# Kernel optimization log

Hardware: AMD Instinct MI355X
Metric: run time of the kernel (lower is better)

## Reference

```python
import jax, jax.numpy as jnp
import numpy as np

B, S, H, NH, HD = 2, 2048, 2048, 16, 128
E, TOPK, I = 8, 2, 2048
EPS = 1e-5
ROPE_THETA = 10000.0


def setup_inputs() -> dict:
    key = jax.random.key(0)
    ks = jax.random.split(key, 11)
    s = 0.02
    return {
        "hidden_states": jax.random.normal(ks[0], (B, S, H), jnp.float32),
        "position_ids": jnp.broadcast_to(jnp.arange(S, dtype=jnp.int32), (B, S)),
        "rms1_w": jnp.ones((H,), jnp.float32),
        "rms2_w": jnp.ones((H,), jnp.float32),
        "q_w": jax.random.normal(ks[1], (H, H), jnp.float32) * s,
        "k_w": jax.random.normal(ks[2], (H, H), jnp.float32) * s,
        "v_w": jax.random.normal(ks[3], (H, H), jnp.float32) * s,
        "o_w": jax.random.normal(ks[4], (H, H), jnp.float32) * s,
        "router_w": jax.random.normal(ks[5], (H, E), jnp.float32) * s,
        "w1": jax.random.normal(ks[6], (E, H, I), jnp.float32) * s,
        "w2": jax.random.normal(ks[7], (E, I, H), jnp.float32) * s,
        "w3": jax.random.normal(ks[8], (E, H, I), jnp.float32) * s,
    }


def rmsnorm(x, w):
    var = jnp.mean(x * x, axis=-1, keepdims=True)
    return (x * jax.lax.rsqrt(var + EPS)) * w


def rope(x, pos):
    # x: [B,S,NH,HD], pos: [B,S]
    half = HD // 2
    inv_freq = 1.0 / (ROPE_THETA ** (jnp.arange(0, half, dtype=jnp.float32) / half))
    ang = pos.astype(jnp.float32)[..., None] * inv_freq  # [B,S,half]
    cos = jnp.cos(ang)[:, :, None, :]
    sin = jnp.sin(ang)[:, :, None, :]
    x1, x2 = x[..., :half], x[..., half:]
    return jnp.concatenate([x1 * cos - x2 * sin, x2 * cos + x1 * sin], axis=-1)


def attention(x, pos, q_w, k_w, v_w, o_w):
    q = (x @ q_w).reshape(B, S, NH, HD)
    k = (x @ k_w).reshape(B, S, NH, HD)
    v = (x @ v_w).reshape(B, S, NH, HD)
    q = rope(q, pos)
    k = rope(k, pos)
    scores = jnp.einsum("bqhd,bkhd->bhqk", q, k) / np.sqrt(HD).astype(np.float32)
    causal = jnp.tril(jnp.ones((S, S), bool))
    scores = jnp.where(causal, scores, jnp.finfo(scores.dtype).min)
    probs = jax.nn.softmax(scores, axis=-1)
    ctx = jnp.einsum("bhqk,bkhd->bqhd", probs, v).reshape(B, S, H)
    return ctx @ o_w


def moe(x, router_w, w1, w2, w3):
    t = x.reshape(B * S, H)
    probs = jax.nn.softmax(t @ router_w, axis=-1)  # [T,E]
    top_v, top_i = jax.lax.top_k(probs, TOPK)
    top_v = top_v / jnp.sum(top_v, axis=-1, keepdims=True)
    T = B * S
    coeff = jnp.zeros((T, E), x.dtype).at[jnp.arange(T)[:, None], top_i].set(top_v)
    y = jnp.zeros((T, H), x.dtype)
    for e in range(E):  # fixed small expert loop
        h = jax.nn.silu(t @ w1[e]) * (t @ w3[e])
        y = y + coeff[:, e:e + 1] * (h @ w2[e])
    return y.reshape(B, S, H)


def reference(hidden_states, position_ids, rms1_w, rms2_w, q_w, k_w, v_w, o_w,
              router_w, w1, w2, w3):
    residual = hidden_states
    h = rmsnorm(hidden_states, rms1_w).astype(hidden_states.dtype)
    h = attention(h, position_ids, q_w, k_w, v_w, o_w)
    h = residual + h
    residual = h
    h = rmsnorm(h, rms2_w).astype(h.dtype)
    h = moe(h, router_w, w1, w2, w3)
    return residual + h
```

## Files before the change

kernel.cpp:

```cpp
#include <hip/hip_runtime.h>
#include <hip/hip_bf16.h>

constexpr int CB   = 2;
constexpr int CS   = 2048;
constexpr int CH   = 2048;
constexpr int CNH  = 16;
constexpr int CHD  = 128;
constexpr int CE   = 8;
constexpr int CI   = 2048;
constexpr int CT   = CB * CS;
constexpr int CQK  = 4096;

typedef __attribute__((ext_vector_type(8))) short short8;
typedef __attribute__((ext_vector_type(4))) float float4v;
typedef __attribute__((ext_vector_type(4))) unsigned short ushort4v;
typedef unsigned int uint32;

__device__ __forceinline__ float bf2f(unsigned short u) {
    union { unsigned int i; float f; } x; x.i = ((unsigned int)u) << 16; return x.f;
}
__device__ __forceinline__ unsigned short f2bf(float f) {
    union { float f; unsigned int i; } x; x.f = f;
    unsigned int r = x.i + 0x7fffu + ((x.i >> 16) & 1u);
    return (unsigned short)(r >> 16);
}
__device__ __forceinline__ uint32 packpair(uint32 r0, uint32 r1) {
    return __builtin_amdgcn_perm(r1, r0, 0x07060302u);
}
__device__ __forceinline__ uint32 rnebits(float f) {
    uint32 u = __float_as_uint(f);
    return u + 0x7fffu + ((u >> 16) & 1u);
}
__device__ __forceinline__ void split2(float f0, float f1, uint32& h, uint32& l) {
    uint32 r0 = rnebits(f0), r1 = rnebits(f1);
    h = packpair(r0, r1);
    float d0 = f0 - __uint_as_float(r0 & 0xffff0000u);
    float d1 = f1 - __uint_as_float(r1 & 0xffff0000u);
    l = packpair(rnebits(d0), rnebits(d1));
}
__device__ __forceinline__ void rne16_store(const float* fv, unsigned short* dst) {
    uint32 h[8];
    #pragma unroll
    for (int p = 0; p < 8; p++) h[p] = packpair(rnebits(fv[2 * p]), rnebits(fv[2 * p + 1]));
    ((uint4*)dst)[0] = make_uint4(h[0], h[1], h[2], h[3]);
    ((uint4*)dst)[1] = make_uint4(h[4], h[5], h[6], h[7]);
}
__device__ __forceinline__ void gl16(const void* g, void* l) {
    __builtin_amdgcn_global_load_lds(
        (const __attribute__((address_space(1))) void*)g,
        (__attribute__((address_space(3))) void*)l, 16, 0, 0);
}

__global__ __launch_bounds__(256) void rmsnorm_k(const float* __restrict__ x,
                                                 const float* __restrict__ w,
                                                 unsigned short* __restrict__ o1,
                                                 unsigned short* __restrict__ o2) {
    const int row = blockIdx.x;
    const float* xr = x + (size_t)row * CH;
    const int base = threadIdx.x * 8;
    float4 v0 = *(const float4*)(xr + base);
    float4 v1 = *(const float4*)(xr + base + 4);
    float ss = v0.x*v0.x + v0.y*v0.y + v0.z*v0.z + v0.w*v0.w
             + v1.x*v1.x + v1.y*v1.y + v1.z*v1.z + v1.w*v1.w;
    #pragma unroll
    for (int o = 1; o < 64; o <<= 1) ss += __shfl_xor(ss, o);
    __shared__ float ps[4];
    if ((threadIdx.x & 63) == 0) ps[threadIdx.x >> 6] = ss;
    __syncthreads();
    const float scale = rsqrtf((ps[0] + ps[1] + ps[2] + ps[3]) / (float)CH + 1e-5f);
    float4 w0 = *(const float4*)(w + base);
    float4 w1 = *(const float4*)(w + base + 4);
    float r[8] = {v0.x * scale * w0.x, v0.y * scale * w0.y, v0.z * scale * w0.z, v0.w * scale * w0.w,
                  v1.x * scale * w1.x, v1.y * scale * w1.y, v1.z * scale * w1.z, v1.w * scale * w1.w};
    uint32 h[4], l[4];
    #pragma unroll
    for (int p = 0; p < 4; p++) split2(r[2 * p], r[2 * p + 1], h[p], l[p]);
    *(uint4*)(o1 + (size_t)row * CH + base) = make_uint4(h[0], h[1], h[2], h[3]);
    *(uint4*)(o2 + (size_t)row * CH + base) = make_uint4(l[0], l[1], l[2], l[3]);
}

__global__ __launch_bounds__(256) void rmsrouter_k(const float* __restrict__ x,
                                                   const float* __restrict__ w,
                                                   const float* __restrict__ rw,
                                                   unsigned short* __restrict__ h2,
                                                   int* __restrict__ cnt,
                                                   int* __restrict__ tok,
                                                   float* __restrict__ gate) {
    const int row = blockIdx.x;
    const float* xr = x + (size_t)row * CH;
    const int base = threadIdx.x * 8;
    float4 v0 = *(const float4*)(xr + base);
    float4 v1 = *(const float4*)(xr + base + 4);
    float ss = v0.x*v0.x + v0.y*v0.y + v0.z*v0.z + v0.w*v0.w
             + v1.x*v1.x + v1.y*v1.y + v1.z*v1.z + v1.w*v1.w;
    #pragma unroll
    for (int o = 1; o < 64; o <<= 1) ss += __shfl_xor(ss, o);
    __shared__ float ps[4];
    __shared__ double dacc[4][8];
    const int wave = threadIdx.x >> 6, lane = threadIdx.x & 63;
    if (lane == 0) ps[wave] = ss;
    __syncthreads();
    const float scale = rsqrtf((ps[0] + ps[1] + ps[2] + ps[3]) / (float)CH + 1e-5f);
    float4 w0 = *(const float4*)(w + base);
    float4 w1 = *(const float4*)(w + base + 4);
    float r[8] = {v0.x * scale * w0.x, v0.y * scale * w0.y, v0.z * scale * w0.z, v0.w * scale * w0.w,
                  v1.x * scale * w1.x, v1.y * scale * w1.y, v1.z * scale * w1.z, v1.w * scale * w1.w};
    rne16_store(r, h2 + (size_t)row * CH + base);
    const float vv[8] = {v0.x, v0.y, v0.z, v0.w, v1.x, v1.y, v1.z, v1.w};
    const float ww[8] = {w0.x, w0.y, w0.z, w0.w, w1.x, w1.y, w1.z, w1.w};
    double acc[8] = {0, 0, 0, 0, 0, 0, 0, 0};
    #pragma unroll
    for (int jj = 0; jj < 8; jj++) {
        const double xn = (double)vv[jj] * (double)ww[jj];
        const float* rr = rw + (size_t)(base + jj) * CE;
        #pragma unroll
        for (int e = 0; e < 8; e++) acc[e] += xn * (double)rr[e];
    }
    #pragma unroll
    for (int e = 0; e < 8; e++) {
        #pragma unroll
        for (int o = 1; o < 64; o <<= 1) acc[e] += __shfl_xor(acc[e], o);
    }
    if (lane == 0) {
        #pragma unroll
        for (int e = 0; e < 8; e++) dacc[wave][e] = acc[e];
    }
    __syncthreads();
    if (threadIdx.x == 0) {
        double a[8];
        #pragma unroll
        for (int e = 0; e < 8; e++) a[e] = dacc[0][e] + dacc[1][e] + dacc[2][e] + dacc[3][e];
        int e0 = 0;
        #pragma unroll
        for (int e = 1; e < 8; e++) if (a[e] > a[e0]) e0 = e;
        int e1 = (e0 == 0) ? 1 : 0;
        #pragma unroll
        for (int e = 0; e < 8; e++) if (e != e0 && a[e] > a[e1]) e1 = e;
        const double dl = (double)scale * (a[e1] - a[e0]);
        const double p1r = exp(dl);
        const float g0 = (float)(1.0 / (1.0 + p1r));
        const float g1 = (float)(p1r / (1.0 + p1r));
        int pos0 = atomicAdd(&cnt[e0], 1);
        tok[e0 * 4096 + pos0] = row; gate[e0 * 4096 + pos0] = g0;
        int pos1 = atomicAdd(&cnt[e1], 1);
        tok[e1 * 4096 + pos1] = row; gate[e1 * 4096 + pos1] = g1;
    }
}

__global__ void rope_tab_k(float2* __restrict__ tab) {
    int i = blockIdx.x * 256 + threadIdx.x;
    int p = i >> 6, j = i & 63;
    double inv = pow(10000.0, -(double)j / 64.0);
    float invf = (float)inv;
    float angf = (float)p * invf;
    double da = (double)angf;
    tab[i] = make_float2((float)cos(da), (float)sin(da));
}

__global__ __launch_bounds__(256) void rope_k(unsigned short* __restrict__ qh,
                                              unsigned short* __restrict__ ql,
                                              const int* __restrict__ pos,
                                              const float2* __restrict__ tab) {
    int i = blockIdx.x * 256 + threadIdx.x;
    if (i >= CT * CNH * 8) return;
    int t = i >> 7, r = i & 127, hh = r >> 3, jo = (r & 7) << 3;
    const float2* tp = tab + (size_t)pos[t] * 64 + jo;
    float4 tc0 = ((const float4*)tp)[0];
    float4 tc1 = ((const float4*)tp)[1];
    float4 tc2 = ((const float4*)tp)[2];
    float4 tc3 = ((const float4*)tp)[3];
    float cx[8] = {tc0.x, tc0.z, tc1.x, tc1.z, tc2.x, tc2.z, tc3.x, tc3.z};
    float cy[8] = {tc0.y, tc0.w, tc1.y, tc1.w, tc2.y, tc2.w, tc3.y, tc3.w};
    const size_t off = (size_t)t * CQK + hh * CHD + jo;
    #pragma unroll
    for (int s = 0; s < 2; s++) {
        unsigned short* hp = qh + off + s * CH;
        unsigned short* lp = ql + off + s * CH;
        short8 x1h = *(short8*)hp,        x1l = *(short8*)lp;
        short8 x2h = *(short8*)(hp + 64), x2l = *(short8*)(lp + 64);
        const unsigned short* p1h = (const unsigned short*)&x1h;
        const unsigned short* p1l = (const unsigned short*)&x1l;
        const unsigned short* p2h = (const unsigned short*)&x2h;
        const unsigned short* p2l = (const unsigned short*)&x2l;
        short8 y1h, y1l, y2h, y2l;
        unsigned short* q1h = (unsigned short*)&y1h;
        unsigned short* q1l = (unsigned short*)&y1l;
        unsigned short* q2h = (unsigned short*)&y2h;
        unsigned short* q2l = (unsigned short*)&y2l;
        #pragma unroll
        for (int jj = 0; jj < 8; jj++) {
            const float x1 = bf2f(p1h[jj]) + bf2f(p1l[jj]);
            const float x2 = bf2f(p2h[jj]) + bf2f(p2l[jj]);
            const float yy1 = x1 * cx[jj] - x2 * cy[jj];
            const float yy2 = x2 * cx[jj] + x1 * cy[jj];
            const uint32 r1 = rnebits(yy1), r2 = rnebits(yy2);
            q1h[jj] = (unsigned short)(r1 >> 16);
            q2h[jj] = (unsigned short)(r2 >> 16);
            q1l[jj] = f2bf(yy1 - __uint_as_float(r1 & 0xffff0000u));
            q2l[jj] = f2bf(yy2 - __uint_as_float(r2 & 0xffff0000u));
        }
        *(short8*)hp        = y1h;
        *(short8*)(hp + 64) = y2h;
        *(short8*)lp        = y1l;
        *(short8*)(lp + 64) = y2l;
    }
}

template<int NMAT>
__global__ __launch_bounds__(256) void conv_k(const float* __restrict__ S0,
                                              const float* __restrict__ S1,
                                              unsigned short* __restrict__ D) {
    __shared__ float t[64][65];
    const int n0 = blockIdx.x * 64, k0 = blockIdx.y * 64, e = blockIdx.z;
    const size_t esrc = (size_t)e * 2048 * 2048;
    const int cc = threadIdx.x & 63, r4 = threadIdx.x >> 6;
    const int nl = threadIdx.x >> 2, q = threadIdx.x & 3;
    #pragma unroll
    for (int s = 0; s < NMAT; s++) {
        const float* S = s ? S1 : S0;
        __syncthreads();
        #pragma unroll
        for (int j = 0; j < 16; j++) {
            const int row = j * 4 + r4;
            t[cc][row] = S[esrc + (size_t)(k0 + row) * 2048 + n0 + cc];
        }
        __syncthreads();
        const int orow = (NMAT == 2) ? (2 * (n0 + nl) + s) : (n0 + nl);
        unsigned short* dp = D + (size_t)e * (NMAT * 2048) * 2048 + (size_t)orow * 2048 + k0 + q * 16;
        float fv[16];
        #pragma unroll
        for (int j = 0; j < 16; j++) fv[j] = t[nl][q * 16 + j];
        rne16_store(fv, dp);
    }
}

template<int NMAT>
__global__ __launch_bounds__(256) void convs_k(const float* __restrict__ S0,
                                               const float* __restrict__ S1,
                                               const float* __restrict__ S2,
                                               unsigned short* __restrict__ Dh,
                                               unsigned short* __restrict__ Dl) {
    __shared__ float t[64][65];
    const int n0 = blockIdx.x * 64, k0 = blockIdx.y * 64, z = blockIdx.z;
    const float* S = S0;
    if (NMAT == 3) S = (z == 0) ? S0 : ((z == 1) ? S1 : S2);
    const int cc = threadIdx.x & 63, r4 = threadIdx.x >> 6;
    #pragma unroll
    for (int j = 0; j < 16; j++) {
        const int row = j * 4 + r4;
        t[cc][row] = S[(size_t)(k0 + row) * 2048 + n0 + cc];
    }
    __syncthreads();
    const int nl = threadIdx.x >> 2, q = threadIdx.x & 3;
    float fv[16];
    #pragma unroll
    for (int j = 0; j < 16; j++) fv[j] = t[nl][q * 16 + j];
    uint32 h[8], l[8];
    #pragma unroll
    for (int p = 0; p < 8; p++) split2(fv[2 * p], fv[2 * p + 1], h[p], l[p]);
    const size_t off = (size_t)(z * 2048 + n0 + nl) * 2048 + k0 + q * 16;
    ((uint4*)(Dh + off))[0] = make_uint4(h[0], h[1], h[2], h[3]);
    ((uint4*)(Dh + off))[1] = make_uint4(h[4], h[5], h[6], h[7]);
    ((uint4*)(Dl + off))[0] = make_uint4(l[0], l[1], l[2], l[3]);
    ((uint4*)(Dl + off))[1] = make_uint4(l[4], l[5], l[6], l[7]);
}

template<int MODE>
__global__ __launch_bounds__(256) void sgemm_k(
    const unsigned short* __restrict__ Ahg, const unsigned short* __restrict__ Alg, int lda,
    const unsigned short* __restrict__ Bhg, const unsigned short* __restrict__ Blg, int K,
    unsigned short* __restrict__ Ch, unsigned short* __restrict__ Cl,
    float* __restrict__ Cf, int ldc,
    const float* __restrict__ resid, float* __restrict__ C2,
    unsigned short* __restrict__ Vh, unsigned short* __restrict__ Vl) {
    __shared__ unsigned short SS[2][4][128 * 32];
    const int mt = blockIdx.x, nt = blockIdx.y, tid = threadIdx.x;
    const int m0 = mt * 128;
    const int wave = tid >> 6, lane = tid & 63;
    const int lr = lane & 15, lg = lane >> 4;
    const int wr = (tid >> 7) & 1, wc = (tid >> 6) & 1;
    const int sr = lane >> 2;
    const int sc = (lane & 3) * 8;
    const int r0 = wave * 32;
    const int lofs = r0 * 32;
    const unsigned short* gAh = Ahg + (size_t)(m0 + r0 + sr) * lda + sc;
    const unsigned short* gAl = Alg + (size_t)(m0 + r0 + sr) * lda + sc;
    const unsigned short* gBh = Bhg + (size_t)(nt * 128 + r0 + sr) * K + sc;
    const unsigned short* gBl = Blg + (size_t)(nt * 128 + r0 + sr) * K + sc;
    const size_t rstepA = (size_t)16 * lda, rstepB = (size_t)16 * K;

    float4v acc[4][4];
    #pragma unroll
    for (int m = 0; m < 4; m++)
        #pragma unroll
        for (int n = 0; n < 4; n++) acc[m][n] = (float4v){0.f, 0.f, 0.f, 0.f};

    gl16(gAh, &SS[0][0][lofs]);           gl16(gAh + rstepA, &SS[0][0][lofs + 512]);
    gl16(gAl, &SS[0][1][lofs]);           gl16(gAl + rstepA, &SS[0][1][lofs + 512]);
    gl16(gBh, &SS[0][2][lofs]);           gl16(gBh + rstepB, &SS[0][2][lofs + 512]);
    gl16(gBl, &SS[0][3][lofs]);           gl16(gBl + rstepB, &SS[0][3][lofs + 512]);
    __syncthreads();

    int cur = 0;
    for (int k0 = 0; k0 < K; k0 += 32) {
        if (k0 + 32 < K) {
            const int nb = cur ^ 1;
            const int kn = k0 + 32;
            gl16(gAh + kn, &SS[nb][0][lofs]);          gl16(gAh + kn + rstepA, &SS[nb][0][lofs + 512]);
            gl16(gAl + kn, &SS[nb][1][lofs]);          gl16(gAl + kn + rstepA, &SS[nb][1][lofs + 512]);
            gl16(gBh + kn, &SS[nb][2][lofs]);          gl16(gBh + kn + rstepB, &SS[nb][2][lofs + 512]);
            gl16(gBl + kn, &SS[nb][3][lofs]);          gl16(gBl + kn + rstepB, &SS[nb][3][lofs + 512]);
        }
        const unsigned short* PAh = SS[cur][0];
        const unsigned short* PAl = SS[cur][1];
        const unsigned short* PBh = SS[cur][2];
        const unsigned short* PBl = SS[cur][3];
        short8 fah[4], fal[4], fbh[4], fbl[4];
        #pragma unroll
        for (int m = 0; m < 4; m++) {
            fah[m] = *(const short8*)(PAh + (wr * 64 + m * 16 + lr) * 32 + lg * 8);
            fal[m] = *(const short8*)(PAl + (wr * 64 + m * 16 + lr) * 32 + lg * 8);
        }
        #pragma unroll
        for (int n = 0; n < 4; n++) {
            fbh[n] = *(const short8*)(PBh + (wc * 64 + n * 16 + lr) * 32 + lg * 8);
            fbl[n] = *(const short8*)(PBl + (wc * 64 + n * 16 + lr) * 32 + lg * 8);
        }
        #pragma unroll
        for (int n = 0; n < 4; n++)
            #pragma unroll
            for (int m = 0; m < 4; m++) {
                acc[m][n] = __builtin_amdgcn_mfma_f32_16x16x32_bf16(fal[m], fbh[n], acc[m][n], 0, 0, 0);
                acc[m][n] = __builtin_amdgcn_mfma_f32_16x16x32_bf16(fah[m], fbl[n], acc[m][n], 0, 0, 0);
                acc[m][n] = __builtin_amdgcn_mfma_f32_16x16x32_bf16(fah[m], fbh[n], acc[m][n], 0, 0, 0);
            }
        __syncthreads();
        cur ^= 1;
    }
    if (MODE == 0 && nt >= 32) {
        #pragma unroll
        for (int m = 0; m < 4; m++) {
            const int rb = wr * 64 + m * 16 + lg * 4;
            #pragma unroll
            for (int n = 0; n < 4; n++) {
                const int vcol = nt * 128 + wc * 64 + n * 16 + lr - 4096;
                ushort4v wh4, wl4;
                #pragma unroll
                for (int r = 0; r < 4; r++) {
                    const float v = acc[m][n][r];
                    uint32 rr = rnebits(v);
                    wh4[r] = (unsigned short)(rr >> 16);
                    wl4[r] = f2bf(v - __uint_as_float(rr & 0xffff0000u));
                }
                *(ushort4v*)(Vh + (size_t)vcol * (size_t)CT + (m0 + rb)) = wh4;
                *(ushort4v*)(Vl + (size_t)vcol * (size_t)CT + (m0 + rb)) = wl4;
            }
        }
        return;
    }
    #pragma unroll
    for (int m = 0; m < 4; m++) {
        const int rb = wr * 64 + m * 16 + lg * 4;
        #pragma unroll
        for (int n = 0; n < 4; n++) {
            const int ccol = nt * 128 + wc * 64 + n * 16 + lr;
            #pragma unroll
            for (int r = 0; r < 4; r++) {
                const size_t idx = (size_t)(m0 + rb + r) * ldc + ccol;
                if (MODE == 1) {
                    const float v = acc[m][n][r] + resid[idx];
                    Cf[idx] = v;
                    C2[idx] = v;
                } else {
                    const float v = acc[m][n][r];
                    uint32 rr = rnebits(v);
                    Ch[idx] = (unsigned short)(rr >> 16);
                    Cl[idx] = f2bf(v - __uint_as_float(rr & 0xffff0000u));
                }
            }
        }
    }
}

template<int MODE>
__global__ __launch_bounds__(256) void gemm_k(
    const unsigned short* __restrict__ A, int lda,
    const unsigned short* __restrict__ Bt, int K, int Ne,
    void* __restrict__ Cp, int ldc,
    const int* __restrict__ cnt, const int* __restrict__ tokl,
    const float* __restrict__ gatel, const int* __restrict__ pb) {
    __shared__ unsigned short SS[2][2][128 * 32];
    const int nt = blockIdx.x, mt = blockIdx.y, e = blockIdx.z;
    const int m0 = mt * 128;
    const int c = cnt[e];
    if (m0 >= c) return;
    const int valid = (c - m0 < 128) ? (c - m0) : 128;
    const int tid = threadIdx.x;
    const int wave = tid >> 6, lane = tid & 63;
    const int lr = lane & 15;
    const int wr = (tid >> 7) & 1, wc = (tid >> 6) & 1;
    const int sr = lane >> 2, sc = (lane & 3) * 8;
    const int r0 = wave * 32;
    const int lofs = r0 * 32;
    size_t gr0, gr1;
    {
        int ra = r0 + sr, rb2 = r0 + 16 + sr;
        if (MODE == 2) {
            ra = ra < valid ? ra : valid - 1;
            rb2 = rb2 < valid ? rb2 : valid - 1;
            gr0 = (size_t)tokl[e * 4096 + m0 + ra];
            gr1 = (size_t)tokl[e * 4096 + m0 + rb2];
        } else {
            int x0 = m0 + ra, x1 = m0 + rb2;
            gr0 = (size_t)(pb[e] + (x0 < c ? x0 : c - 1));
            gr1 = (size_t)(pb[e] + (x1 < c ? x1 : c - 1));
        }
    }
    const unsigned short* gA0 = A + gr0 * (size_t)lda + sc;
    const unsigned short* gA1 = A + gr1 * (size_t)lda + sc;
    const unsigned short* gB = Bt + (size_t)e * Ne * K + (size_t)(nt * 128 + r0 + sr) * K + sc;
    const size_t rstepB = (size_t)16 * K;

    float4v acc[4][4];
    #pragma unroll
    for (int m = 0; m < 4; m++)
        #pragma unroll
        for (int n = 0; n < 4; n++) acc[m][n] = (float4v){0.f, 0.f, 0.f, 0.f};

    gl16(gA0, &SS[0][0][lofs]);           gl16(gA1, &SS[0][0][lofs + 512]);
    gl16(gB, &SS[0][1][lofs]);            gl16(gB + rstepB, &SS[0][1][lofs + 512]);
    __syncthreads();

    int cur = 0;
    for (int k0 = 0; k0 < K; k0 += 32) {
        if (k0 + 32 < K) {
            const int nb = cur ^ 1;
            const int kn = k0 + 32;
            gl16(gA0 + kn, &SS[nb][0][lofs]);          gl16(gA1 + kn, &SS[nb][0][lofs + 512]);
            gl16(gB + kn, &SS[nb][1][lofs]);           gl16(gB + kn + rstepB, &SS[nb][1][lofs + 512]);
        }
        const unsigned short* PA = SS[cur][0];
        const unsigned short* PB = SS[cur][1];
        short8 af[4], bf[4];
        const int lg = lane >> 4;
        #pragma unroll
        for (int m = 0; m < 4; m++) af[m] = *(const short8*)(PA + (wr * 64 + m * 16 + lr) * 32 + lg * 8);
        #pragma unroll
        for (int n = 0; n < 4; n++) bf[n] = *(const short8*)(PB + (wc * 64 + n * 16 + lr) * 32 + lg * 8);
        #pragma unroll
        for (int n = 0; n < 4; n++)
            #pragma unroll
            for (int m = 0; m < 4; m++)
                acc[m][n] = __builtin_amdgcn_mfma_f32_16x16x32_bf16(af[m], bf[n], acc[m][n], 0, 0, 0);
        __syncthreads();
        cur ^= 1;
    }

    #pragma unroll
    for (int m = 0; m < 4; m++) {
        const int rb = wr * 64 + m * 16 + (lane >> 4) * 4;
        #pragma unroll
        for (int n = 0; n < 4; n++) {
            const int col = nt * 128 + wc * 64 + n * 16 + lr;
            #pragma unroll
            for (int r = 0; r < 4; r++) {
                const int row = rb + r;
                const float v = acc[m][n][r];
                if (MODE == 2) {
                    const float other = __shfl_xor(v, 1);
                    if (!(lr & 1) && row < valid) {
                        const float g1 = v, g3 = other;
                        const float hsw = (g1 / (1.f + __expf(-g1))) * g3;
                        ((unsigned short*)Cp)[(size_t)(pb[e] + m0 + row) * ldc + (col >> 1)] = f2bf(hsw);
                    }
                } else {
                    if (row < valid) {
                        const int t = tokl[e * 4096 + m0 + row];
                        const float g = gatel[e * 4096 + m0 + row];
                        atomicAdd(((float*)Cp) + (size_t)t * ldc + col, v * g);
                    }
                }
            }
        }
    }
}

__global__ __launch_bounds__(256) void attn_k(const unsigned short* __restrict__ qkh,
                                              const unsigned short* __restrict__ qkl,
                                              const unsigned short* __restrict__ vth,
                                              const unsigned short* __restrict__ vtl,
                                              unsigned short* __restrict__ ch,
                                              unsigned short* __restrict__ cl) {
    __shared__ unsigned short Kb[2][2][32][136];
    __shared__ unsigned short Vb[2][2][128 * 32];
    const int bid = blockIdx.x;
    const int xcd = bid & 7, jj = bid >> 3;
    const int bh  = xcd * 4 + (jj >> 5);
    const int qb  = 31 - (jj & 31);
    const int h   = bh & 15, b = bh >> 4;
    const int tid = threadIdx.x;
    const int wave = tid >> 6, lane = tid & 63, lr = lane & 15, lg = lane >> 4;
    const size_t tb = (size_t)b * CS;
    const int q0 = qb * 64 + wave * 16;

    short8 qfh[4], qfl[4];
    {
        const size_t off = (tb + q0 + lr) * CQK + h * CHD;
        #pragma unroll
        for (int c = 0; c < 4; c++) {
            qfh[c] = *(const short8*)(qkh + off + c * 32 + lg * 8);
            qfl[c] = *(const short8*)(qkl + off + c * 32 + lg * 8);
        }
    }
    float4v o[8];
    #pragma unroll
    for (int d = 0; d < 8; d++) o[d] = (float4v){0.f, 0.f, 0.f, 0.f};
    float m = -1e30f, l = 0.f;
    const float scl = 0.08838834764831845f;
    const int ntiles = 2 * (qb + 1);
    const int kk = tid >> 3, slot = tid & 7;

    short8 kh0, kh1, kl0, kl1;
    const size_t vrow = (size_t)(h * 128 + wave * 32 + (lane >> 2));
    const unsigned short* gV0 = vth + vrow * (size_t)CT + tb + (lane & 3) * 8;
    const unsigned short* gV1 = vtl + vrow * (size_t)CT + tb + (lane & 3) * 8;

    #define LOADK(KV0) { \
        const size_t koff = (tb + (KV0) + kk) * CQK + CH + h * CHD + slot * 16; \
        kh0 = *(const short8*)(qkh + koff);     kh1 = *(const short8*)(qkh + koff + 8); \
        kl0 = *(const short8*)(qkl + koff);     kl1 = *(const short8*)(qkl + koff + 8); }
    #define WRITEK(BUF) { \
        *(short8*)(&Kb[BUF][0][kk][slot * 16])     = kh0; \
        *(short8*)(&Kb[BUF][0][kk][slot * 16 + 8]) = kh1; \
        *(short8*)(&Kb[BUF][1][kk][slot * 16])     = kl0; \
        *(short8*)(&Kb[BUF][1][kk][slot * 16 + 8]) = kl1; }
    #define ISSUEV(BUF, KV0) { \
        gl16(gV0 + (KV0), &Vb[BUF][0][wave * 32 * 32]); \
        gl16(gV0 + (KV0) + (size_t)16 * CT, &Vb[BUF][0][wave * 32 * 32 + 512]); \
        gl16(gV1 + (KV0), &Vb[BUF][1][wave * 32 * 32]); \
        gl16(gV1 + (KV0) + (size_t)16 * CT, &Vb[BUF][1][wave * 32 * 32 + 512]); }

    LOADK(0);
    WRITEK(0);
    ISSUEV(0, 0);
    LOADK(32);
    __syncthreads();

    int cur = 0;
    for (int kt = 0; kt < ntiles; ++kt) {
        const int kv0 = kt * 32;
        if (kt + 1 < ntiles) {
            WRITEK(cur ^ 1);
            ISSUEV(cur ^ 1, kv0 + 32);
        }
        if (kt + 2 < ntiles) LOADK(kv0 + 64);

        const unsigned short* KH = &Kb[cur][0][0][0];
        const unsigned short* KL = &Kb[cur][1][0][0];
        const unsigned short* VH = Vb[cur][0];
        const unsigned short* VL = Vb[cur][1];

        float4v st0 = (float4v){0.f,0.f,0.f,0.f}, st1 = st0;
        #pragma unroll
        for (int c = 0; c < 4; c++) {
            short8 kah = *(const short8*)(KH + lr * 136 + c * 32 + lg * 8);
            short8 kal = *(const short8*)(KL + lr * 136 + c * 32 + lg * 8);
            short8 kbh = *(const short8*)(KH + (16 + lr) * 136 + c * 32 + lg * 8);
            short8 kbl = *(const short8*)(KL + (16 + lr) * 136 + c * 32 + lg * 8);
            st0 = __builtin_amdgcn_mfma_f32_16x16x32_bf16(kal, qfh[c], st0, 0, 0, 0);
            st0 = __builtin_amdgcn_mfma_f32_16x16x32_bf16(kah, qfl[c], st0, 0, 0, 0);
            st0 = __builtin_amdgcn_mfma_f32_16x16x32_bf16(kah, qfh[c], st0, 0, 0, 0);
            st1 = __builtin_amdgcn_mfma_f32_16x16x32_bf16(kbl, qfh[c], st1, 0, 0, 0);
            st1 = __builtin_amdgcn_mfma_f32_16x16x32_bf16(kbh, qfl[c], st1, 0, 0, 0);
            st1 = __builtin_amdgcn_mfma_f32_16x16x32_bf16(kbh, qfh[c], st1, 0, 0, 0);
        }
        float pv[8]; float pmax = -1e30f;
        const int qg = q0 + lr;
        #pragma unroll
        for (int f = 0; f < 2; f++) {
            #pragma unroll
            for (int r = 0; r < 4; r++) {
                const int kg = kv0 + f * 16 + lg * 4 + r;
                const float s = (kg <= qg) ? ((f ? st1[r] : st0[r]) * scl) : -1e30f;
                pv[f * 4 + r] = s;
                pmax = fmaxf(pmax, s);
            }
        }
        pmax = fmaxf(pmax, __shfl_xor(pmax, 16));
        pmax = fmaxf(pmax, __shfl_xor(pmax, 32));
        if (!__all(pmax <= m)) {
            const float mnew = fmaxf(m, pmax);
            const float alpha = __expf(m - mnew);
            l *= alpha;
            #pragma unroll
            for (int d = 0; d < 8; d++) o[d] *= alpha;
            m = mnew;
        }
        float sum = 0.f;
        #pragma unroll
        for (int i = 0; i < 8; i++) { const float p = __expf(pv[i] - m); pv[i] = p; sum += p; }
        sum += __shfl_xor(sum, 16);
        sum += __shfl_xor(sum, 32);
        l += sum;
        short8 pfh, pfl;
        unsigned short* pfhp = (unsigned short*)&pfh;
        unsigned short* pflp = (unsigned short*)&pfl;
        #pragma unroll
        for (int j = 0; j < 8; j++) {
            const int srcl = (((lg & 1) * 2 + (j >> 2)) << 4) | lr;
            const float a0 = __shfl(pv[j & 3], srcl);
            const float a1 = __shfl(pv[4 + (j & 3)], srcl);
            const float sel = (lg >= 2) ? a1 : a0;
            uint32 r = rnebits(sel);
            pfhp[j] = (unsigned short)(r >> 16);
            float d = sel - __uint_as_float(r & 0xffff0000u);
            pflp[j] = (unsigned short)(rnebits(d) >> 16);
        }
        #pragma unroll
        for (int dt = 0; dt < 8; dt++) {
            short8 vh = *(const short8*)(VH + (dt * 16 + lr) * 32 + lg * 8);
            short8 vl = *(const short8*)(VL + (dt * 16 + lr) * 32 + lg * 8);
            o[dt] = __builtin_amdgcn_mfma_f32_16x16x32_bf16(vl, pfh, o[dt], 0, 0, 0);
            o[dt] = __builtin_amdgcn_mfma_f32_16x16x32_bf16(vh, pfl, o[dt], 0, 0, 0);
            o[dt] = __builtin_amdgcn_mfma_f32_16x16x32_bf16(vh, pfh, o[dt], 0, 0, 0);
        }
        __syncthreads();
        cur ^= 1;
    }
    #undef LOADK
    #undef WRITEK
    #undef ISSUEV
    const float inv = 1.f / l;
    const size_t coff = (tb + q0 + lr) * CH + h * CHD + lg * 4;
    #pragma unroll
    for (int dt = 0; dt < 8; dt++) {
        ushort4v wh, wl;
        #pragma unroll
        for (int r = 0; r < 4; r++) {
            const float v = o[dt][r] * inv;
            uint32 rr = rnebits(v);
            wh[r] = (unsigned short)(rr >> 16);
            wl[r] = f2bf(v - __uint_as_float(rr & 0xffff0000u));
        }
        *(ushort4v*)(ch + coff + dt * 16) = wh;
        *(ushort4v*)(cl + coff + dt * 16) = wl;
    }
}

__global__ void prefix_k(const int* __restrict__ cnt, int* __restrict__ pb) {
    if (threadIdx.x == 0 && blockIdx.x == 0) {
        int s = 0;
        for (int e = 0; e < CE; e++) { pb[e] = s; s += cnt[e]; }
    }
}

extern "C" void kernel_launch(void* const* d_in, const int* in_sizes, int n_in,
                              void* d_out, int out_size, void* d_ws, size_t ws_size,
                              hipStream_t stream) {
    (void)in_sizes; (void)n_in; (void)out_size; (void)ws_size;
    const float* hidden = (const float*)d_in[0];
    const int*   posids = (const int*)d_in[1];
    const float* rms1w  = (const float*)d_in[2];
    const float* rms2w  = (const float*)d_in[3];
    const float* qw     = (const float*)d_in[4];
    const float* kw     = (const float*)d_in[5];
    const float* vw     = (const float*)d_in[6];
    const float* ow     = (const float*)d_in[7];
    const float* rw     = (const float*)d_in[8];
    const float* w1     = (const float*)d_in[9];
    const float* w2     = (const float*)d_in[10];
    const float* w3     = (const float*)d_in[11];
    float* out = (float*)d_out;

    char* ws = (char*)d_ws;
    unsigned short* h1h = (unsigned short*)ws;
    unsigned short* h1l = (unsigned short*)(ws + 16777216);
    unsigned short* woh = (unsigned short*)ws;
    unsigned short* wol = (unsigned short*)(ws + 8388608);
    unsigned short* h2  = (unsigned short*)ws;
    int*   tok  = (int*)(ws + 16777216);
    float* gate = (float*)(ws + 16777216 + 131072);
    int*   cnt  = (int*)(ws + 16777216 + 262144);
    int*   pb   = cnt + 16;
    unsigned short* qkh = (unsigned short*)(ws + 33554432);
    unsigned short* qkl = (unsigned short*)(ws + 67108864);
    unsigned short* vth = (unsigned short*)(ws + 100663296);
    unsigned short* vtl = (unsigned short*)(ws + 117440512);
    unsigned short* wt13 = (unsigned short*)(ws + 33554432);
    unsigned short* wt2  = (unsigned short*)(ws + 33554432);
    unsigned short* wqkvh = (unsigned short*)(ws + 134217728);
    unsigned short* wqkvl = (unsigned short*)(ws + 134217728 + 25165824);
    unsigned short* ctxh = (unsigned short*)(ws + 134217728);
    unsigned short* ctxl = (unsigned short*)(ws + 150994944);
    float*          res2 = (float*)(ws + 167772160);
    unsigned short* Hbuf = (unsigned short*)(ws + 167772160);
    float2*         rtab = (float2*)(ws + 201326592);

    rope_tab_k<<<512, 256, 0, stream>>>(rtab);
    rmsnorm_k<<<CT, 256, 0, stream>>>(hidden, rms1w, h1h, h1l);
    convs_k<3><<<dim3(32, 32, 3), 256, 0, stream>>>(qw, kw, vw, wqkvh, wqkvl);
    sgemm_k<0><<<dim3(32, 48), 256, 0, stream>>>(h1h, h1l, CH, wqkvh, wqkvl, CH,
                                                 qkh, qkl, nullptr, CQK, nullptr, nullptr,
                                                 vth, vtl);
    rope_k<<<2048, 256, 0, stream>>>(qkh, qkl, posids, rtab);
    convs_k<1><<<dim3(32, 32, 1), 256, 0, stream>>>(ow, nullptr, nullptr, woh, wol);
    attn_k<<<1024, 256, 0, stream>>>(qkh, qkl, vth, vtl, ctxh, ctxl);
    sgemm_k<1><<<dim3(32, 16), 256, 0, stream>>>(ctxh, ctxl, CH, woh, wol, CH,
                                                 nullptr, nullptr, res2, CH, hidden, out,
                                                 nullptr, nullptr);
    hipMemsetAsync(cnt, 0, 8 * sizeof(int), stream);
    rmsrouter_k<<<CT, 256, 0, stream>>>(res2, rms2w, rw, h2, cnt, tok, gate);
    prefix_k<<<1, 64, 0, stream>>>(cnt, pb);
    conv_k<2><<<dim3(32, 32, CE), 256, 0, stream>>>(w1, w3, wt13);
    gemm_k<2><<<dim3(32, 32, CE), 256, 0, stream>>>(h2, CH, wt13, CH, 2 * CI, Hbuf, CI,
                                                    cnt, tok, gate, pb);
    conv_k<1><<<dim3(32, 32, CE), 256, 0, stream>>>(w2, nullptr, wt2);
    gemm_k<3><<<dim3(16, 32, CE), 256, 0, stream>>>(Hbuf, CI, wt2, CI, CH, out, CH,
                                                    cnt, tok, gate, pb);
}
```

Before: 1.286 ms.

## Fuse RoPE into QKV GEMM epilogue and load MoE A-operand directly to registers

Q and K weight rows are permuted during conversion so rotary pairs sit in adjacent columns. The RoPE rotation then runs in the QKV GEMM epilogue using a lane-shuffle partner, and the separate rope kernel is removed. That saves a full read-modify-write pass over the Q/K hi/lo buffers. Separately, the MoE gather GEMM now loads the gathered A rows straight from global memory into registers, prefetched one step ahead, instead of staging them in shared memory. This halves LDS use but may give less coalesced gathered loads and higher register pressure.

After: 1.498 ms. 16.5% more time.

```diff
diff --git a/kernel.cpp b/kernel.cpp
--- a/kernel.cpp
+++ b/kernel.cpp
@@ -157,55 +157,6 @@
     tab[i] = make_float2((float)cos(da), (float)sin(da));
 }
 
-__global__ __launch_bounds__(256) void rope_k(unsigned short* __restrict__ qh,
-                                              unsigned short* __restrict__ ql,
-                                              const int* __restrict__ pos,
-                                              const float2* __restrict__ tab) {
-    int i = blockIdx.x * 256 + threadIdx.x;
-    if (i >= CT * CNH * 8) return;
-    int t = i >> 7, r = i & 127, hh = r >> 3, jo = (r & 7) << 3;
-    const float2* tp = tab + (size_t)pos[t] * 64 + jo;
-    float4 tc0 = ((const float4*)tp)[0];
-    float4 tc1 = ((const float4*)tp)[1];
-    float4 tc2 = ((const float4*)tp)[2];
-    float4 tc3 = ((const float4*)tp)[3];
-    float cx[8] = {tc0.x, tc0.z, tc1.x, tc1.z, tc2.x, tc2.z, tc3.x, tc3.z};
-    float cy[8] = {tc0.y, tc0.w, tc1.y, tc1.w, tc2.y, tc2.w, tc3.y, tc3.w};
-    const size_t off = (size_t)t * CQK + hh * CHD + jo;
-    #pragma unroll
-    for (int s = 0; s < 2; s++) {
-        unsigned short* hp = qh + off + s * CH;
-        unsigned short* lp = ql + off + s * CH;
-        short8 x1h = *(short8*)hp,        x1l = *(short8*)lp;
-        short8 x2h = *(short8*)(hp + 64), x2l = *(short8*)(lp + 64);
-        const unsigned short* p1h = (const unsigned short*)&x1h;
-        const unsigned short* p1l = (const unsigned short*)&x1l;
-        const unsigned short* p2h = (const unsigned short*)&x2h;
-        const unsigned short* p2l = (const unsigned short*)&x2l;
-        short8 y1h, y1l, y2h, y2l;
-        unsigned short* q1h = (unsigned short*)&y1h;
-        unsigned short* q1l = (unsigned short*)&y1l;
-        unsigned short* q2h = (unsigned short*)&y2h;
-        unsigned short* q2l = (unsigned short*)&y2l;
-        #pragma unroll
-        for (int jj = 0; jj < 8; jj++) {
-            const float x1 = bf2f(p1h[jj]) + bf2f(p1l[jj]);
-            const float x2 = bf2f(p2h[jj]) + bf2f(p2l[jj]);
-            const float yy1 = x1 * cx[jj] - x2 * cy[jj];
-            const float yy2 = x2 * cx[jj] + x1 * cy[jj];
-            const uint32 r1 = rnebits(yy1), r2 = rnebits(yy2);
-            q1h[jj] = (unsigned short)(r1 >> 16);
-            q2h[jj] = (unsigned short)(r2 >> 16);
-            q1l[jj] = f2bf(yy1 - __uint_as_float(r1 & 0xffff0000u));
-            q2l[jj] = f2bf(yy2 - __uint_as_float(r2 & 0xffff0000u));
-        }
-        *(short8*)hp        = y1h;
-        *(short8*)(hp + 64) = y2h;
-        *(short8*)lp        = y1l;
-        *(short8*)(lp + 64) = y2l;
-    }
-}
-
 template<int NMAT>
 __global__ __launch_bounds__(256) void conv_k(const float* __restrict__ S0,
                                               const float* __restrict__ S1,
@@ -258,7 +209,16 @@
     uint32 h[8], l[8];
     #pragma unroll
     for (int p = 0; p < 8; p++) split2(fv[2 * p], fv[2 * p + 1], h[p], l[p]);
-    const size_t off = (size_t)(z * 2048 + n0 + nl) * 2048 + k0 + q * 16;
+    int orow;
+    const int gcol = n0 + nl;
+    if (NMAT == 3 && z < 2) {
+        const int head = gcol >> 7, dd = gcol & 127;
+        const int nd = (dd < 64) ? (2 * dd) : (2 * (dd - 64) + 1);
+        orow = z * 2048 + head * 128 + nd;
+    } else {
+        orow = z * 2048 + gcol;
+    }
+    const size_t off = (size_t)orow * 2048 + k0 + q * 16;
     ((uint4*)(Dh + off))[0] = make_uint4(h[0], h[1], h[2], h[3]);
     ((uint4*)(Dh + off))[1] = make_uint4(h[4], h[5], h[6], h[7]);
     ((uint4*)(Dl + off))[0] = make_uint4(l[0], l[1], l[2], l[3]);
@@ -272,7 +232,8 @@
     unsigned short* __restrict__ Ch, unsigned short* __restrict__ Cl,
     float* __restrict__ Cf, int ldc,
     const float* __restrict__ resid, float* __restrict__ C2,
-    unsigned short* __restrict__ Vh, unsigned short* __restrict__ Vl) {
+    unsigned short* __restrict__ Vh, unsigned short* __restrict__ Vl,
+    const int* __restrict__ posids, const float2* __restrict__ rtab) {
     __shared__ unsigned short SS[2][4][128 * 32];
     const int mt = blockIdx.x, nt = blockIdx.y, tid = threadIdx.x;
     const int m0 = mt * 128;
@@ -358,6 +319,31 @@
         }
         return;
     }
+    if (MODE == 0) {
+        #pragma unroll
+        for (int m = 0; m < 4; m++) {
+            const int rb = wr * 64 + m * 16 + lg * 4;
+            #pragma unroll
+            for (int n = 0; n < 4; n++) {
+                const int ccol = nt * 128 + wc * 64 + n * 16 + lr;
+                const int j = (wc * 64 + n * 16 + lr) >> 1;
+                #pragma unroll
+                for (int r = 0; r < 4; r++) {
+                    const int row = m0 + rb + r;
+                    const float v = acc[m][n][r];
+                    const float partner = __shfl_xor(v, 1);
+                    const float2 cs = rtab[(size_t)posids[row] * 64 + j];
+                    const float y = (lr & 1) ? (v * cs.x + partner * cs.y)
+                                             : (v * cs.x - partner * cs.y);
+                    const size_t idx = (size_t)row * ldc + ccol;
+                    uint32 rr = rnebits(y);
+                    Ch[idx] = (unsigned short)(rr >> 16);
+                    Cl[idx] = f2bf(y - __uint_as_float(rr & 0xffff0000u));
+                }
+            }
+        }
+        return;
+    }
     #pragma unroll
     for (int m = 0; m < 4; m++) {
         const int rb = wr * 64 + m * 16 + lg * 4;
@@ -367,16 +353,9 @@
             #pragma unroll
             for (int r = 0; r < 4; r++) {
                 const size_t idx = (size_t)(m0 + rb + r) * ldc + ccol;
-                if (MODE == 1) {
-                    const float v = acc[m][n][r] + resid[idx];
-                    Cf[idx] = v;
-                    C2[idx] = v;
-                } else {
-                    const float v = acc[m][n][r];
-                    uint32 rr = rnebits(v);
-                    Ch[idx] = (unsigned short)(rr >> 16);
-                    Cl[idx] = f2bf(v - __uint_as_float(rr & 0xffff0000u));
-                }
+                const float v = acc[m][n][r] + resid[idx];
+                Cf[idx] = v;
+                C2[idx] = v;
             }
         }
     }
@@ -389,7 +368,7 @@
     void* __restrict__ Cp, int ldc,
     const int* __restrict__ cnt, const int* __restrict__ tokl,
     const float* __restrict__ gatel, const int* __restrict__ pb) {
-    __shared__ unsigned short SS[2][2][128 * 32];
+    __shared__ unsigned short BS[2][128 * 32];
     const int nt = blockIdx.x, mt = blockIdx.y, e = blockIdx.z;
     const int m0 = mt * 128;
     const int c = cnt[e];
@@ -397,29 +376,27 @@
     const int valid = (c - m0 < 128) ? (c - m0) : 128;
     const int tid = threadIdx.x;
     const int wave = tid >> 6, lane = tid & 63;
-    const int lr = lane & 15;
+    const int lr = lane & 15, lg = lane >> 4;
     const int wr = (tid >> 7) & 1, wc = (tid >> 6) & 1;
     const int sr = lane >> 2, sc = (lane & 3) * 8;
     const int r0 = wave * 32;
     const int lofs = r0 * 32;
-    size_t gr0, gr1;
-    {
-        int ra = r0 + sr, rb2 = r0 + 16 + sr;
-        if (MODE == 2) {
-            ra = ra < valid ? ra : valid - 1;
-            rb2 = rb2 < valid ? rb2 : valid - 1;
-            gr0 = (size_t)tokl[e * 4096 + m0 + ra];
-            gr1 = (size_t)tokl[e * 4096 + m0 + rb2];
-        } else {
-            int x0 = m0 + ra, x1 = m0 + rb2;
-            gr0 = (size_t)(pb[e] + (x0 < c ? x0 : c - 1));
-            gr1 = (size_t)(pb[e] + (x1 < c ? x1 : c - 1));
-        }
-    }
-    const unsigned short* gA0 = A + gr0 * (size_t)lda + sc;
-    const unsigned short* gA1 = A + gr1 * (size_t)lda + sc;
     const unsigned short* gB = Bt + (size_t)e * Ne * K + (size_t)(nt * 128 + r0 + sr) * K + sc;
     const size_t rstepB = (size_t)16 * K;
+    const unsigned short* aP[4];
+    #pragma unroll
+    for (int m = 0; m < 4; m++) {
+        const int row = wr * 64 + m * 16 + lr;
+        size_t gr;
+        if (MODE == 2) {
+            const int idx = m0 + (row < valid ? row : valid - 1);
+            gr = (size_t)tokl[e * 4096 + idx];
+        } else {
+            const int x = m0 + row;
+            gr = (size_t)(pb[e] + (x < c ? x : c - 1));
+        }
+        aP[m] = A + gr * (size_t)lda + lg * 8;
+    }
 
     float4v acc[4][4];
     #pragma unroll
@@ -427,38 +404,44 @@
         #pragma unroll
         for (int n = 0; n < 4; n++) acc[m][n] = (float4v){0.f, 0.f, 0.f, 0.f};
 
-    gl16(gA0, &SS[0][0][lofs]);           gl16(gA1, &SS[0][0][lofs + 512]);
-    gl16(gB, &SS[0][1][lofs]);            gl16(gB + rstepB, &SS[0][1][lofs + 512]);
+    gl16(gB, &BS[0][lofs]);
+    gl16(gB + rstepB, &BS[0][lofs + 512]);
+    short8 afc[4];
+    #pragma unroll
+    for (int m = 0; m < 4; m++) afc[m] = *(const short8*)(aP[m]);
     __syncthreads();
 
     int cur = 0;
     for (int k0 = 0; k0 < K; k0 += 32) {
-        if (k0 + 32 < K) {
+        short8 afn[4];
+        const bool more = (k0 + 32 < K);
+        if (more) {
             const int nb = cur ^ 1;
-            const int kn = k0 + 32;
-            gl16(gA0 + kn, &SS[nb][0][lofs]);          gl16(gA1 + kn, &SS[nb][0][lofs + 512]);
-            gl16(gB + kn, &SS[nb][1][lofs]);           gl16(gB + kn + rstepB, &SS[nb][1][lofs + 512]);
-        }
-        const unsigned short* PA = SS[cur][0];
-        const unsigned short* PB = SS[cur][1];
-        short8 af[4], bf[4];
-        const int lg = lane >> 4;
-        #pragma unroll
-        for (int m = 0; m < 4; m++) af[m] = *(const short8*)(PA + (wr * 64 + m * 16 + lr) * 32 + lg * 8);
+            gl16(gB + k0 + 32, &BS[nb][lofs]);
+            gl16(gB + k0 + 32 + rstepB, &BS[nb][lofs + 512]);
+            #pragma unroll
+            for (int m = 0; m < 4; m++) afn[m] = *(const short8*)(aP[m] + k0 + 32);
+        }
+        const unsigned short* PB = BS[cur];
+        short8 bf[4];
         #pragma unroll
         for (int n = 0; n < 4; n++) bf[n] = *(const short8*)(PB + (wc * 64 + n * 16 + lr) * 32 + lg * 8);
         #pragma unroll
         for (int n = 0; n < 4; n++)
             #pragma unroll
             for (int m = 0; m < 4; m++)
-                acc[m][n] = __builtin_amdgcn_mfma_f32_16x16x32_bf16(af[m], bf[n], acc[m][n], 0, 0, 0);
+                acc[m][n] = __builtin_amdgcn_mfma_f32_16x16x32_bf16(afc[m], bf[n], acc[m][n], 0, 0, 0);
         __syncthreads();
+        if (more) {
+            #pragma unroll
+            for (int m = 0; m < 4; m++) afc[m] = afn[m];
+        }
         cur ^= 1;
     }
 
     #pragma unroll
     for (int m = 0; m < 4; m++) {
-        const int rb = wr * 64 + m * 16 + (lane >> 4) * 4;
+        const int rb = wr * 64 + m * 16 + lg * 4;
         #pragma unroll
         for (int n = 0; n < 4; n++) {
             const int col = nt * 128 + wc * 64 + n * 16 + lr;
@@ -701,13 +684,12 @@
     convs_k<3><<<dim3(32, 32, 3), 256, 0, stream>>>(qw, kw, vw, wqkvh, wqkvl);
     sgemm_k<0><<<dim3(32, 48), 256, 0, stream>>>(h1h, h1l, CH, wqkvh, wqkvl, CH,
                                                  qkh, qkl, nullptr, CQK, nullptr, nullptr,
-                                                 vth, vtl);
-    rope_k<<<2048, 256, 0, stream>>>(qkh, qkl, posids, rtab);
+                                                 vth, vtl, posids, rtab);
     convs_k<1><<<dim3(32, 32, 1), 256, 0, stream>>>(ow, nullptr, nullptr, woh, wol);
     attn_k<<<1024, 256, 0, stream>>>(qkh, qkl, vth, vtl, ctxh, ctxl);
     sgemm_k<1><<<dim3(32, 16), 256, 0, stream>>>(ctxh, ctxl, CH, woh, wol, CH,
                                                  nullptr, nullptr, res2, CH, hidden, out,
-                                                 nullptr, nullptr);
+                                                 nullptr, nullptr, nullptr, nullptr);
     hipMemsetAsync(cnt, 0, 8 * sizeof(int), stream);
     rmsrouter_k<<<CT, 256, 0, stream>>>(res2, rms2w, rw, h2, cnt, tok, gate);
     prefix_k<<<1, 64, 0, stream>>>(cnt, pb);
```
